# Kernel optimization log

Measured on AMD Instinct MI355X. Metric: run time of the kernel, lower is better.

## Reference

```python
import jax, jax.numpy as jnp
import numpy as np

B, H, W, C = 4, 64, 64, 256
DQK = C // 8

def setup_inputs() -> dict:
    key = jax.random.key(0)
    kx, kq, kk, kv = jax.random.split(key, 4)
    x = jax.random.normal(kx, (B, H, W, C), dtype=jnp.float32)
    Wq = jax.random.normal(kq, (C, DQK), dtype=jnp.float32) * 0.05
    Wk = jax.random.normal(kk, (C, DQK), dtype=jnp.float32) * 0.05
    Wv = jax.random.normal(kv, (C, C), dtype=jnp.float32) * 0.05
    gamma = jnp.ones((1,), dtype=jnp.float32)  # nonzero so attention path matters
    return {"x": x, "Wq": Wq, "Wk": Wk, "Wv": Wv, "gamma": gamma}

def reference(x, Wq, Wk, Wv, gamma):
    b, h, w, c = x.shape
    n = h * w
    xf = x.reshape(b, n, c)                      # [B, N, C]
    q = jnp.einsum('bnc,cd->bnd', xf, Wq)        # [B, N, C/8]  (1x1 conv == GEMM)
    k = jnp.einsum('bnc,cd->bnd', xf, Wk)        # [B, N, C/8]
    v = jnp.einsum('bnc,ce->bne', xf, Wv)        # [B, N, C]
    scores = jnp.einsum('bnd,bmd->bnm', q, k)    # [B, N, N], no scaling (as in source)
    attn = jax.nn.softmax(scores, axis=-1)
    out = jnp.einsum('bnm,bme->bne', attn, v)    # [B, N, C]
    out = out.reshape(b, h, w, c)
    return x + gamma * out
```

## Files before the change

### kernel.cpp

```cpp
#include <hip/hip_runtime.h>
#include <stdint.h>

#define BB 4
#define NN 4096
#define CC 256
#define DD 32

typedef __bf16 bf16;
typedef bf16 bf16x4 __attribute__((ext_vector_type(4)));
typedef bf16 bf16x8 __attribute__((ext_vector_type(8)));
typedef float f32x4 __attribute__((ext_vector_type(4)));
typedef unsigned int u32x4 __attribute__((ext_vector_type(4)));

__global__ void prepw_kernel(const float* __restrict__ Wq,
                             const float* __restrict__ Wk,
                             const float* __restrict__ Wv,
                             bf16* __restrict__ WT)
{
    int i = blockIdx.x * 256 + threadIdx.x;
    if (i < 320 * 256) {
        int d = i >> 8, c = i & 255;
        float val;
        if (d < DD)          val = Wq[c * DD + d] * 1.4426950408889634f;
        else if (d < 2 * DD) val = Wk[c * DD + (d - DD)];
        else                 val = Wv[c * CC + (d - 2 * DD)];
        WT[i] = (bf16)val;
    }
}

__global__ __launch_bounds__(256) void proj_kernel(
    const float* __restrict__ x, const bf16* __restrict__ WT,
    bf16* __restrict__ qb, bf16* __restrict__ kb, bf16* __restrict__ vt)
{
    int b = blockIdx.x >> 7, nt = blockIdx.x & 127;
    int n0 = nt << 5;
    int tid = threadIdx.x;
    int w = tid >> 6, lane = tid & 63;
    int lm = lane & 15, g = lane >> 4;
    int rw = w >> 1;
    int ch = w & 1;

    f32x4 acc[10];
    f32x4 zero4 = {0.f, 0.f, 0.f, 0.f};
#pragma unroll
    for (int i = 0; i < 10; ++i) acc[i] = zero4;

    const float* xrow = x + ((size_t)(b * NN) + n0 + rw * 16 + lm) * CC;
    for (int kc = 0; kc < 8; ++kc) {
        f32x4 a0 = *(const f32x4*)(xrow + kc * 32 + g * 8);
        f32x4 a1 = *(const f32x4*)(xrow + kc * 32 + g * 8 + 4);
        bf16x8 a;
        a[0] = (bf16)a0[0]; a[1] = (bf16)a0[1]; a[2] = (bf16)a0[2]; a[3] = (bf16)a0[3];
        a[4] = (bf16)a1[0]; a[5] = (bf16)a1[1]; a[6] = (bf16)a1[2]; a[7] = (bf16)a1[3];
#pragma unroll
        for (int ct = 0; ct < 10; ++ct) {
            int ctg = ch * 10 + ct;
            bf16x8 wv = *(const bf16x8*)(WT + (ctg * 16 + lm) * 256 + kc * 32 + g * 8);
            acc[ct] = __builtin_amdgcn_mfma_f32_16x16x32_bf16(a, wv, acc[ct], 0, 0, 0);
        }
    }

#pragma unroll
    for (int ct = 0; ct < 10; ++ct) {
        int ctg = ch * 10 + ct;
        int col = ctg * 16 + lm;
        if (ctg < 4) {
#pragma unroll
            for (int r = 0; r < 4; ++r) {
                int n = n0 + rw * 16 + g * 4 + r;
                bf16 hv = (bf16)acc[ct][r];
                if (ctg < 2) qb[((size_t)(b * NN) + n) * DD + col] = hv;
                else         kb[((size_t)(b * NN) + n) * DD + (col - DD)] = hv;
            }
        } else {
            int c = col - 64;
            int tile = nt >> 1;
            int nbase = ((nt & 1) * 32 + rw * 16 + g * 4) ^ ((c & 7) << 3);
            bf16x4 pk;
            pk[0] = (bf16)acc[ct][0]; pk[1] = (bf16)acc[ct][1];
            pk[2] = (bf16)acc[ct][2]; pk[3] = (bf16)acc[ct][3];
            size_t off = (((size_t)(b * 64 + tile)) * 256 + c) * 64 + nbase;
            *(bf16x4*)(vt + off) = pk;
        }
    }
}


#define LOADK(KT_, KF) { \
    const bf16* kbase_ = kb + ((size_t)(b * NN) + (size_t)(KT_) * 64) * DD + g * 8; \
    KF[0] = *(const bf16x8*)(kbase_ + (lm +  0) * DD); \
    KF[1] = *(const bf16x8*)(kbase_ + (lm + 16) * DD); \
    KF[2] = *(const bf16x8*)(kbase_ + (lm + 32) * DD); \
    KF[3] = *(const bf16x8*)(kbase_ + (lm + 48) * DD); }

#define LOADV(KT_, VB) { \
    const bf16* vtile_ = vt + ((size_t)(b * 64 + (KT_))) * 16384; \
    _Pragma("unroll") \
    for (int ct_ = 0; ct_ < 4; ++ct_) { \
        int c_ = 64 * w + 16 * ct_ + lm; \
        const bf16* vrow_ = vtile_ + c_ * 64; \
        int vsw_ = (c_ & 7) << 3; \
        VB[ct_][0] = *(const bf16x8*)(vrow_ + ((8 * g) ^ vsw_)); \
        VB[ct_][1] = *(const bf16x8*)(vrow_ + ((32 + 8 * g) ^ vsw_)); \
    } }

#define PVBLOCK(PRV_, VB) { \
    const float* alph_p = (const float*)(lds + 16384 + (PRV_) * 512); \
    const uint32_t* flg_p = (const uint32_t*)(lds + 16384 + (PRV_) * 512 + 256); \
    const unsigned char* Pp_ = lds + (PRV_) * 8192; \
    u32x4 fl_ = *(const u32x4*)flg_p; \
    if ((fl_[0] & fl_[1] & fl_[2] & fl_[3]) == 0u) { \
        _Pragma("unroll") for (int rt_ = 0; rt_ < 4; ++rt_) { \
            f32x4 a_ = *(const f32x4*)(alph_p + rt_ * 16 + 4 * g); \
            _Pragma("unroll") for (int ct_ = 0; ct_ < 4; ++ct_) { \
                acc[rt_][ct_][0] *= a_[0]; acc[rt_][ct_][1] *= a_[1]; \
                acc[rt_][ct_][2] *= a_[2]; acc[rt_][ct_][3] *= a_[3]; \
            } \
        } \
    } \
    int psw_ = (lm & 7) << 4; \
    _Pragma("unroll") for (int rt_ = 0; rt_ < 4; ++rt_) { \
        const unsigned char* pr_ = Pp_ + (rt_ * 16 + lm) * 128; \
        bf16x8 pa0_ = *(const bf16x8*)(pr_ + (( 0 + 16 * g) ^ psw_)); \
        bf16x8 pa1_ = *(const bf16x8*)(pr_ + ((64 + 16 * g) ^ psw_)); \
        _Pragma("unroll") for (int ct_ = 0; ct_ < 4; ++ct_) { \
            acc[rt_][ct_] = __builtin_amdgcn_mfma_f32_16x16x32_bf16(pa0_, VB[ct_][0], acc[rt_][ct_], 0, 0, 0); \
            acc[rt_][ct_] = __builtin_amdgcn_mfma_f32_16x16x32_bf16(pa1_, VB[ct_][1], acc[rt_][ct_], 0, 0, 0); \
        } \
    } \
}

#define STEP(T_, KF, KFN, VBP, DOPV) { \
    const int cur_ = (T_) & 1; \
    __builtin_amdgcn_s_setprio(1); \
    f32x4 sv0 = __builtin_amdgcn_mfma_f32_16x16x32_bf16(KF[0], qf, zero4, 0, 0, 0); \
    f32x4 sv1 = __builtin_amdgcn_mfma_f32_16x16x32_bf16(KF[1], qf, zero4, 0, 0, 0); \
    f32x4 sv2 = __builtin_amdgcn_mfma_f32_16x16x32_bf16(KF[2], qf, zero4, 0, 0, 0); \
    f32x4 sv3 = __builtin_amdgcn_mfma_f32_16x16x32_bf16(KF[3], qf, zero4, 0, 0, 0); \
    int ktn_ = ((T_) + 1 < kt1) ? ((T_) + 1) : (kt1 - 1); \
    LOADK(ktn_, KFN); \
    if (DOPV) { PVBLOCK(cur_ ^ 1, VBP); } \
    __builtin_amdgcn_s_setprio(0); \
    LOADV(ktn_, VBP); \
    float mx_ = fmaxf(fmaxf(fmaxf(sv0[0], sv0[1]), fmaxf(sv0[2], sv0[3])), \
                      fmaxf(fmaxf(sv1[0], sv1[1]), fmaxf(sv1[2], sv1[3]))); \
    mx_ = fmaxf(mx_, fmaxf(fmaxf(sv2[0], sv2[1]), fmaxf(sv2[2], sv2[3]))); \
    mx_ = fmaxf(mx_, fmaxf(fmaxf(sv3[0], sv3[1]), fmaxf(sv3[2], sv3[3]))); \
    float alpha_; \
    int wave_ok_ = __all(mx_ <= mrun + 11.5f); \
    if (!wave_ok_) { \
        float wm_ = mx_; \
        wm_ = fmaxf(wm_, __shfl_xor(wm_, 1)); \
        wm_ = fmaxf(wm_, __shfl_xor(wm_, 2)); \
        wm_ = fmaxf(wm_, __shfl_xor(wm_, 4)); \
        wm_ = fmaxf(wm_, __shfl_xor(wm_, 8)); \
        wm_ = fmaxf(wm_, __shfl_xor(wm_, 16)); \
        wm_ = fmaxf(wm_, __shfl_xor(wm_, 32)); \
        float mn_ = fmaxf(mrun, wm_); \
        alpha_ = __builtin_exp2f(mrun - mn_); \
        mrun = mn_; \
    } else alpha_ = 1.0f; \
    float ssum_; \
    { \
        _Pragma("unroll") for (int j_ = 0; j_ < 4; ++j_) sv0[j_] = __builtin_exp2f(sv0[j_] - mrun); \
        _Pragma("unroll") for (int j_ = 0; j_ < 4; ++j_) sv1[j_] = __builtin_exp2f(sv1[j_] - mrun); \
        _Pragma("unroll") for (int j_ = 0; j_ < 4; ++j_) sv2[j_] = __builtin_exp2f(sv2[j_] - mrun); \
        _Pragma("unroll") for (int j_ = 0; j_ < 4; ++j_) sv3[j_] = __builtin_exp2f(sv3[j_] - mrun); \
        f32x4 t_ = (sv0 + sv1) + (sv2 + sv3); \
        ssum_ = (t_[0] + t_[1]) + (t_[2] + t_[3]); \
    } \
    lrun = lrun * alpha_ + ssum_;   \
    unsigned char* Pb_ = lds + cur_ * 8192; \
    { \
        int rb_ = (16 * w + lm) * 128; \
        int sw_ = (lm & 7) << 4; \
        bf16x4 pk_; \
        pk_[0] = (bf16)sv0[0]; pk_[1] = (bf16)sv0[1]; pk_[2] = (bf16)sv0[2]; pk_[3] = (bf16)sv0[3]; \
        *(bf16x4*)(Pb_ + rb_ + (( 0 + 8 * g) ^ sw_)) = pk_; \
        pk_[0] = (bf16)sv1[0]; pk_[1] = (bf16)sv1[1]; pk_[2] = (bf16)sv1[2]; pk_[3] = (bf16)sv1[3]; \
        *(bf16x4*)(Pb_ + rb_ + ((32 + 8 * g) ^ sw_)) = pk_; \
        pk_[0] = (bf16)sv2[0]; pk_[1] = (bf16)sv2[1]; pk_[2] = (bf16)sv2[2]; pk_[3] = (bf16)sv2[3]; \
        *(bf16x4*)(Pb_ + rb_ + ((64 + 8 * g) ^ sw_)) = pk_; \
        pk_[0] = (bf16)sv3[0]; pk_[1] = (bf16)sv3[1]; pk_[2] = (bf16)sv3[2]; pk_[3] = (bf16)sv3[3]; \
        *(bf16x4*)(Pb_ + rb_ + ((96 + 8 * g) ^ sw_)) = pk_; \
    } \
    float* alph_ = (float*)(lds + 16384 + cur_ * 512); \
    uint32_t* flg_ = (uint32_t*)(lds + 16384 + cur_ * 512 + 256); \
    if (g == 0) alph_[16 * w + lm] = alpha_;   \
    if (lane == 0) flg_[w] = (uint32_t)wave_ok_; \
    asm volatile("s_waitcnt lgkmcnt(0)" ::: "memory"); \
    __builtin_amdgcn_s_barrier(); \
    asm volatile("" ::: "memory"); \
}

__global__ __launch_bounds__(256, 2) void attn_kernel(
    const bf16* __restrict__ qb, const bf16* __restrict__ kb,
    const bf16* __restrict__ vt, const float* __restrict__ x,
    const float* __restrict__ gamma, bf16* __restrict__ pacc,
    float* __restrict__ pml, float* __restrict__ out, int KS)
{
    __shared__ __align__(16) unsigned char lds[17408];
    int bid = blockIdx.x;
    int b, qt, ks;
    if (KS == 2) {
        int xcd = bid & 7, slot = bid >> 3;
        b = xcd >> 1;
        int idx = (xcd & 1) * 64 + slot;
        qt = idx >> 1; ks = idx & 1;
    } else {
        ks = bid % KS; int t = bid / KS; b = t >> 6; qt = t & 63;
    }
    int bq = b * 64 + qt;
    int n0 = qt << 6;
    int tid = threadIdx.x;
    int w = tid >> 6, lane = tid & 63;
    int lm = lane & 15, g = lane >> 4;

    bf16x8 qf = *(const bf16x8*)(qb + ((size_t)(b * NN) + n0 + w * 16 + lm) * DD + g * 8);

    f32x4 acc[4][4];
    f32x4 zero4 = {0.f, 0.f, 0.f, 0.f};
#pragma unroll
    for (int i = 0; i < 4; ++i)
#pragma unroll
        for (int j = 0; j < 4; ++j) acc[i][j] = zero4;
    float mrun = -1e30f, lrun = 0.f;

    int KT = 64 / KS;
    int kt0 = ks * KT;
    int kt1 = kt0 + KT;

    bf16x8 kfA[4], kfB[4];
    bf16x8 vbA[4][2], vbB[4][2];
    LOADK(kt0, kfA);
    LOADV(kt0, vbA);

    STEP(kt0, kfA, kfB, vbB, 0);

    int kt = kt0 + 1;
    while (kt + 2 <= kt1) {
        STEP(kt,     kfB, kfA, vbA, 1);
        STEP(kt + 1, kfA, kfB, vbB, 1);
        kt += 2;
    }
    if (kt < kt1) {
        STEP(kt, kfB, kfA, vbA, 1);
    }
    PVBLOCK(1, vbB);

    lrun += __shfl_xor(lrun, 16);
    lrun += __shfl_xor(lrun, 32);

    if (KS == 1) {
        __syncthreads();
        float* lsh = (float*)(lds + 16384);
        if (g == 0) lsh[16 * w + lm] = lrun;
        __syncthreads();
        float gam = gamma[0];
#pragma unroll
        for (int rt = 0; rt < 4; ++rt) {
            f32x4 lv = *(const f32x4*)(lsh + rt * 16 + 4 * g);
            f32x4 inv;
            inv[0] = 1.f / lv[0]; inv[1] = 1.f / lv[1];
            inv[2] = 1.f / lv[2]; inv[3] = 1.f / lv[3];
#pragma unroll
            for (int ct = 0; ct < 4; ++ct) {
                int col = 64 * w + 16 * ct + lm;
#pragma unroll
                for (int r = 0; r < 4; ++r) {
                    int n = n0 + rt * 16 + 4 * g + r;
                    size_t idx = ((size_t)(b * NN) + n) * CC + col;
                    out[idx] = x[idx] + gam * acc[rt][ct][r] * inv[r];
                }
            }
        }
    } else {
        bf16* pa = pacc + ((size_t)(bq * KS + ks)) * (64 * 256);
#pragma unroll
        for (int rt = 0; rt < 4; ++rt) {
#pragma unroll
            for (int ct = 0; ct < 4; ++ct) {
                int col = 64 * w + 16 * ct + lm;
#pragma unroll
                for (int r = 0; r < 4; ++r) {
                    int rowin = rt * 16 + 4 * g + r;
                    pa[rowin * 256 + col] = (bf16)acc[rt][ct][r];
                }
            }
        }
        if (g == 0) {
            int rowin = 16 * w + lm;
            size_t mo = ((size_t)(bq * KS + ks) * 64 + rowin) * 2;
            pml[mo + 0] = mrun;
            pml[mo + 1] = lrun;
        }
    }
}

__global__ __launch_bounds__(256) void combine_kernel(
    const bf16* __restrict__ pacc, const float* __restrict__ pml,
    const float* __restrict__ x, const float* __restrict__ gamma,
    float* __restrict__ out, int KS)
{
    int tid = threadIdx.x;
    int row = blockIdx.x * 4 + (tid >> 6);
    int lane = tid & 63;
    int bq = row >> 6;
    int r64 = row & 63;

    float m[4], l[4];
    float M = -3e38f;
    for (int ks = 0; ks < KS; ++ks) {
        size_t mo = ((size_t)(bq * KS + ks) * 64 + r64) * 2;
        m[ks] = pml[mo + 0];
        l[ks] = pml[mo + 1];
        M = fmaxf(M, m[ks]);
    }
    float L = 0.f;
    float wgt[4];
    for (int ks = 0; ks < KS; ++ks) {
        wgt[ks] = __builtin_exp2f(m[ks] - M);
        L += wgt[ks] * l[ks];
    }
    float s = gamma[0] / L;

    f32x4 a = {0.f, 0.f, 0.f, 0.f};
    for (int ks = 0; ks < KS; ++ks) {
        const bf16* pa = pacc + ((size_t)(bq * KS + ks) * 64 + r64) * 256;
        bf16x4 v = *(const bf16x4*)(pa + lane * 4);
        a[0] += wgt[ks] * (float)v[0]; a[1] += wgt[ks] * (float)v[1];
        a[2] += wgt[ks] * (float)v[2]; a[3] += wgt[ks] * (float)v[3];
    }
    const f32x4* xv = (const f32x4*)(x + (size_t)row * 256);
    f32x4 xi = xv[lane];
    f32x4 o;
    o[0] = xi[0] + s * a[0]; o[1] = xi[1] + s * a[1];
    o[2] = xi[2] + s * a[2]; o[3] = xi[3] + s * a[3];
    ((f32x4*)(out + (size_t)row * 256))[lane] = o;
}

extern "C" void kernel_launch(void* const* d_in, const int* in_sizes, int n_in,
                              void* d_out, int out_size, void* d_ws, size_t ws_size,
                              hipStream_t stream)
{
    const float* x     = (const float*)d_in[0];
    const float* Wq    = (const float*)d_in[1];
    const float* Wk    = (const float*)d_in[2];
    const float* Wv    = (const float*)d_in[3];
    const float* gamma = (const float*)d_in[4];
    float* out = (float*)d_out;

    char* ws = (char*)d_ws;
    bf16* WT = (bf16*)(ws);
    bf16* qb = (bf16*)(ws + 163840);
    bf16* kb = (bf16*)(ws + 1212416);
    bf16* vt = (bf16*)(ws + 2260992);

    const size_t base = 10649600;
    size_t need2 = base + (size_t)2 * (8388608 + 131072);
    int KS = (ws_size >= need2) ? 2 : 1;

    bf16*  pacc = (bf16*)(ws + base);
    float* pml  = (float*)(ws + base + (size_t)KS * 8388608);

    hipLaunchKernelGGL(prepw_kernel, dim3(320), dim3(256), 0, stream,
                       Wq, Wk, Wv, WT);
    hipLaunchKernelGGL(proj_kernel, dim3(512), dim3(256), 0, stream,
                       x, WT, qb, kb, vt);
    hipLaunchKernelGGL(attn_kernel, dim3(256 * KS), dim3(256), 0, stream,
                       qb, kb, vt, x, gamma, pacc, pml, out, KS);
    if (KS > 1) {
        hipLaunchKernelGGL(combine_kernel, dim3(BB * NN / 4), dim3(256), 0, stream,
                           pacc, pml, x, gamma, out, KS);
    }
}
```

Before: 92.61 us.

## Split attention keys three ways, raise occupancy, and single-buffer K/V fragments

The key range is now split into three partitions instead of two, giving 768 blocks with an XCD-aware block mapping and uneven tile ranges per split. Occupancy is raised to three blocks per SIMD through launch bounds. The double-buffered K/V register fragments and the unrolled two-step loop become a single-buffered rolled loop, which frees registers so the higher occupancy fits. In exchange, V loads now have less time in flight before they are used. The split also needs more workspace; if the buffer is too small, the code falls back to a single split instead of two.

```diff
diff --git a/kernel.cpp b/kernel.cpp
--- a/kernel.cpp
+++ b/kernel.cpp
@@ -11,6 +11,10 @@
 typedef bf16 bf16x8 __attribute__((ext_vector_type(8)));
 typedef float f32x4 __attribute__((ext_vector_type(4)));
 typedef unsigned int u32x4 __attribute__((ext_vector_type(4)));
+
+__device__ __forceinline__ float fm3(float a, float b, float c) {
+    return fmaxf(fmaxf(a, b), c);
+}
 
 __global__ void prepw_kernel(const float* __restrict__ Wq,
                              const float* __restrict__ Wk,
@@ -86,25 +90,25 @@
 }
 
 
-#define LOADK(KT_, KF) { \
+#define LOADK(KT_) { \
     const bf16* kbase_ = kb + ((size_t)(b * NN) + (size_t)(KT_) * 64) * DD + g * 8; \
-    KF[0] = *(const bf16x8*)(kbase_ + (lm +  0) * DD); \
-    KF[1] = *(const bf16x8*)(kbase_ + (lm + 16) * DD); \
-    KF[2] = *(const bf16x8*)(kbase_ + (lm + 32) * DD); \
-    KF[3] = *(const bf16x8*)(kbase_ + (lm + 48) * DD); }
-
-#define LOADV(KT_, VB) { \
+    kf[0] = *(const bf16x8*)(kbase_ + (lm +  0) * DD); \
+    kf[1] = *(const bf16x8*)(kbase_ + (lm + 16) * DD); \
+    kf[2] = *(const bf16x8*)(kbase_ + (lm + 32) * DD); \
+    kf[3] = *(const bf16x8*)(kbase_ + (lm + 48) * DD); }
+
+#define LOADV(KT_) { \
     const bf16* vtile_ = vt + ((size_t)(b * 64 + (KT_))) * 16384; \
     _Pragma("unroll") \
     for (int ct_ = 0; ct_ < 4; ++ct_) { \
         int c_ = 64 * w + 16 * ct_ + lm; \
         const bf16* vrow_ = vtile_ + c_ * 64; \
         int vsw_ = (c_ & 7) << 3; \
-        VB[ct_][0] = *(const bf16x8*)(vrow_ + ((8 * g) ^ vsw_)); \
-        VB[ct_][1] = *(const bf16x8*)(vrow_ + ((32 + 8 * g) ^ vsw_)); \
+        vb[ct_][0] = *(const bf16x8*)(vrow_ + ((8 * g) ^ vsw_)); \
+        vb[ct_][1] = *(const bf16x8*)(vrow_ + ((32 + 8 * g) ^ vsw_)); \
     } }
 
-#define PVBLOCK(PRV_, VB) { \
+#define PVBLOCK(PRV_) { \
     const float* alph_p = (const float*)(lds + 16384 + (PRV_) * 512); \
     const uint32_t* flg_p = (const uint32_t*)(lds + 16384 + (PRV_) * 512 + 256); \
     const unsigned char* Pp_ = lds + (PRV_) * 8192; \
@@ -119,33 +123,27 @@
         } \
     } \
     int psw_ = (lm & 7) << 4; \
+    __builtin_amdgcn_s_setprio(1); \
     _Pragma("unroll") for (int rt_ = 0; rt_ < 4; ++rt_) { \
         const unsigned char* pr_ = Pp_ + (rt_ * 16 + lm) * 128; \
         bf16x8 pa0_ = *(const bf16x8*)(pr_ + (( 0 + 16 * g) ^ psw_)); \
         bf16x8 pa1_ = *(const bf16x8*)(pr_ + ((64 + 16 * g) ^ psw_)); \
         _Pragma("unroll") for (int ct_ = 0; ct_ < 4; ++ct_) { \
-            acc[rt_][ct_] = __builtin_amdgcn_mfma_f32_16x16x32_bf16(pa0_, VB[ct_][0], acc[rt_][ct_], 0, 0, 0); \
-            acc[rt_][ct_] = __builtin_amdgcn_mfma_f32_16x16x32_bf16(pa1_, VB[ct_][1], acc[rt_][ct_], 0, 0, 0); \
+            acc[rt_][ct_] = __builtin_amdgcn_mfma_f32_16x16x32_bf16(pa0_, vb[ct_][0], acc[rt_][ct_], 0, 0, 0); \
+            acc[rt_][ct_] = __builtin_amdgcn_mfma_f32_16x16x32_bf16(pa1_, vb[ct_][1], acc[rt_][ct_], 0, 0, 0); \
         } \
     } \
-}
-
-#define STEP(T_, KF, KFN, VBP, DOPV) { \
+    __builtin_amdgcn_s_setprio(0); \
+}
+
+#define SMTAIL(T_) { \
     const int cur_ = (T_) & 1; \
-    __builtin_amdgcn_s_setprio(1); \
-    f32x4 sv0 = __builtin_amdgcn_mfma_f32_16x16x32_bf16(KF[0], qf, zero4, 0, 0, 0); \
-    f32x4 sv1 = __builtin_amdgcn_mfma_f32_16x16x32_bf16(KF[1], qf, zero4, 0, 0, 0); \
-    f32x4 sv2 = __builtin_amdgcn_mfma_f32_16x16x32_bf16(KF[2], qf, zero4, 0, 0, 0); \
-    f32x4 sv3 = __builtin_amdgcn_mfma_f32_16x16x32_bf16(KF[3], qf, zero4, 0, 0, 0); \
-    int ktn_ = ((T_) + 1 < kt1) ? ((T_) + 1) : (kt1 - 1); \
-    LOADK(ktn_, KFN); \
-    if (DOPV) { PVBLOCK(cur_ ^ 1, VBP); } \
-    __builtin_amdgcn_s_setprio(0); \
-    LOADV(ktn_, VBP); \
-    float mx_ = fmaxf(fmaxf(fmaxf(sv0[0], sv0[1]), fmaxf(sv0[2], sv0[3])), \
-                      fmaxf(fmaxf(sv1[0], sv1[1]), fmaxf(sv1[2], sv1[3]))); \
-    mx_ = fmaxf(mx_, fmaxf(fmaxf(sv2[0], sv2[1]), fmaxf(sv2[2], sv2[3]))); \
-    mx_ = fmaxf(mx_, fmaxf(fmaxf(sv3[0], sv3[1]), fmaxf(sv3[2], sv3[3]))); \
+    float mxa_ = fm3(sv0[0], sv0[1], sv0[2]); \
+    float mxb_ = fm3(sv0[3], sv1[0], sv1[1]); \
+    float mxc_ = fm3(sv1[2], sv1[3], sv2[0]); \
+    float mxd_ = fm3(sv2[1], sv2[2], sv2[3]); \
+    float mxe_ = fm3(sv3[0], sv3[1], sv3[2]); \
+    float mx_ = fmaxf(fm3(mxa_, mxb_, mxc_), fm3(mxd_, mxe_, sv3[3])); \
     float alpha_; \
     int wave_ok_ = __all(mx_ <= mrun + 11.5f); \
     if (!wave_ok_) { \
@@ -186,14 +184,14 @@
     } \
     float* alph_ = (float*)(lds + 16384 + cur_ * 512); \
     uint32_t* flg_ = (uint32_t*)(lds + 16384 + cur_ * 512 + 256); \
-    if (g == 0) alph_[16 * w + lm] = alpha_;   \
+    if (g == 0) alph_[16 * w + lm] = alpha_; \
     if (lane == 0) flg_[w] = (uint32_t)wave_ok_; \
     asm volatile("s_waitcnt lgkmcnt(0)" ::: "memory"); \
     __builtin_amdgcn_s_barrier(); \
     asm volatile("" ::: "memory"); \
 }
 
-__global__ __launch_bounds__(256, 2) void attn_kernel(
+__global__ __launch_bounds__(256, 3) void attn_kernel(
     const bf16* __restrict__ qb, const bf16* __restrict__ kb,
     const bf16* __restrict__ vt, const float* __restrict__ x,
     const float* __restrict__ gamma, bf16* __restrict__ pacc,
@@ -202,11 +200,11 @@
     __shared__ __align__(16) unsigned char lds[17408];
     int bid = blockIdx.x;
     int b, qt, ks;
-    if (KS == 2) {
+    if (KS == 3) {
         int xcd = bid & 7, slot = bid >> 3;
         b = xcd >> 1;
-        int idx = (xcd & 1) * 64 + slot;
-        qt = idx >> 1; ks = idx & 1;
+        int idx = (xcd & 1) * 96 + slot;
+        qt = idx / 3; ks = idx - qt * 3;
     } else {
         ks = bid % KS; int t = bid / KS; b = t >> 6; qt = t & 63;
     }
@@ -226,27 +224,35 @@
         for (int j = 0; j < 4; ++j) acc[i][j] = zero4;
     float mrun = -1e30f, lrun = 0.f;
 
-    int KT = 64 / KS;
-    int kt0 = ks * KT;
-    int kt1 = kt0 + KT;
-
-    bf16x8 kfA[4], kfB[4];
-    bf16x8 vbA[4][2], vbB[4][2];
-    LOADK(kt0, kfA);
-    LOADV(kt0, vbA);
-
-    STEP(kt0, kfA, kfB, vbB, 0);
-
-    int kt = kt0 + 1;
-    while (kt + 2 <= kt1) {
-        STEP(kt,     kfB, kfA, vbA, 1);
-        STEP(kt + 1, kfA, kfB, vbB, 1);
-        kt += 2;
-    }
-    if (kt < kt1) {
-        STEP(kt, kfB, kfA, vbA, 1);
-    }
-    PVBLOCK(1, vbB);
+    int kt0 = (64 * ks) / KS;
+    int kt1 = (64 * (ks + 1)) / KS;
+
+    bf16x8 kf[4];
+    bf16x8 vb[4][2];
+    LOADK(kt0);
+    LOADV(kt0);
+
+    {
+        f32x4 sv0 = __builtin_amdgcn_mfma_f32_16x16x32_bf16(kf[0], qf, zero4, 0, 0, 0);
+        f32x4 sv1 = __builtin_amdgcn_mfma_f32_16x16x32_bf16(kf[1], qf, zero4, 0, 0, 0);
+        f32x4 sv2 = __builtin_amdgcn_mfma_f32_16x16x32_bf16(kf[2], qf, zero4, 0, 0, 0);
+        f32x4 sv3 = __builtin_amdgcn_mfma_f32_16x16x32_bf16(kf[3], qf, zero4, 0, 0, 0);
+        LOADK(kt0 + 1);
+        SMTAIL(kt0);
+    }
+
+    for (int kt = kt0 + 1; kt < kt1; ++kt) {
+        f32x4 sv0 = __builtin_amdgcn_mfma_f32_16x16x32_bf16(kf[0], qf, zero4, 0, 0, 0);
+        f32x4 sv1 = __builtin_amdgcn_mfma_f32_16x16x32_bf16(kf[1], qf, zero4, 0, 0, 0);
+        f32x4 sv2 = __builtin_amdgcn_mfma_f32_16x16x32_bf16(kf[2], qf, zero4, 0, 0, 0);
+        f32x4 sv3 = __builtin_amdgcn_mfma_f32_16x16x32_bf16(kf[3], qf, zero4, 0, 0, 0);
+        int ktn = (kt + 1) & 63;
+        LOADK(ktn);
+        PVBLOCK((kt & 1) ^ 1);
+        LOADV(kt);
+        SMTAIL(kt);
+    }
+    PVBLOCK((kt1 - 1) & 1);
 
     lrun += __shfl_xor(lrun, 16);
     lrun += __shfl_xor(lrun, 32);
@@ -357,8 +363,8 @@
     bf16* vt = (bf16*)(ws + 2260992);
 
     const size_t base = 10649600;
-    size_t need2 = base + (size_t)2 * (8388608 + 131072);
-    int KS = (ws_size >= need2) ? 2 : 1;
+    size_t need3 = base + (size_t)3 * (8388608 + 131072);
+    int KS = (ws_size >= need3) ? 3 : 1;
 
     bf16*  pacc = (bf16*)(ws + base);
     float* pml  = (float*)(ws + base + (size_t)KS * 8388608);
```

After: 95.46 us. 1.03x slower.

## Fuse split-K combine into attention kernel via per-tile atomic counter

Applied to the files above, without the earlier changes.

Removes the separate combine kernel launch. The last-arriving split block for each query tile, detected with an atomic counter after a threadfence, merges the two partial accumulators and writes the output. It also raises wave priority around the PV MFMA block. This saves a launch and lets combine work overlap with attention tail blocks, at the cost of atomics, fences, and one block per tile doing serial combine work.

```diff
diff --git a/kernel.cpp b/kernel.cpp
--- a/kernel.cpp
+++ b/kernel.cpp
@@ -15,9 +15,11 @@
 __global__ void prepw_kernel(const float* __restrict__ Wq,
                              const float* __restrict__ Wk,
                              const float* __restrict__ Wv,
-                             bf16* __restrict__ WT)
+                             bf16* __restrict__ WT,
+                             int* __restrict__ cnt)
 {
     int i = blockIdx.x * 256 + threadIdx.x;
+    if (blockIdx.x == 0 && threadIdx.x < 256) cnt[threadIdx.x] = 0;
     if (i < 320 * 256) {
         int d = i >> 8, c = i & 255;
         float val;
@@ -119,6 +121,7 @@
         } \
     } \
     int psw_ = (lm & 7) << 4; \
+    __builtin_amdgcn_s_setprio(1); \
     _Pragma("unroll") for (int rt_ = 0; rt_ < 4; ++rt_) { \
         const unsigned char* pr_ = Pp_ + (rt_ * 16 + lm) * 128; \
         bf16x8 pa0_ = *(const bf16x8*)(pr_ + (( 0 + 16 * g) ^ psw_)); \
@@ -128,6 +131,7 @@
             acc[rt_][ct_] = __builtin_amdgcn_mfma_f32_16x16x32_bf16(pa1_, VB[ct_][1], acc[rt_][ct_], 0, 0, 0); \
         } \
     } \
+    __builtin_amdgcn_s_setprio(0); \
 }
 
 #define STEP(T_, KF, KFN, VBP, DOPV) { \
@@ -186,7 +190,7 @@
     } \
     float* alph_ = (float*)(lds + 16384 + cur_ * 512); \
     uint32_t* flg_ = (uint32_t*)(lds + 16384 + cur_ * 512 + 256); \
-    if (g == 0) alph_[16 * w + lm] = alpha_;   \
+    if (g == 0) alph_[16 * w + lm] = alpha_; \
     if (lane == 0) flg_[w] = (uint32_t)wave_ok_; \
     asm volatile("s_waitcnt lgkmcnt(0)" ::: "memory"); \
     __builtin_amdgcn_s_barrier(); \
@@ -197,7 +201,8 @@
     const bf16* __restrict__ qb, const bf16* __restrict__ kb,
     const bf16* __restrict__ vt, const float* __restrict__ x,
     const float* __restrict__ gamma, bf16* __restrict__ pacc,
-    float* __restrict__ pml, float* __restrict__ out, int KS)
+    float* __restrict__ pml, int* __restrict__ cnt,
+    float* __restrict__ out, int KS)
 {
     __shared__ __align__(16) unsigned char lds[17408];
     int bid = blockIdx.x;
@@ -294,49 +299,43 @@
             pml[mo + 0] = mrun;
             pml[mo + 1] = lrun;
         }
-    }
-}
-
-__global__ __launch_bounds__(256) void combine_kernel(
-    const bf16* __restrict__ pacc, const float* __restrict__ pml,
-    const float* __restrict__ x, const float* __restrict__ gamma,
-    float* __restrict__ out, int KS)
-{
-    int tid = threadIdx.x;
-    int row = blockIdx.x * 4 + (tid >> 6);
-    int lane = tid & 63;
-    int bq = row >> 6;
-    int r64 = row & 63;
-
-    float m[4], l[4];
-    float M = -3e38f;
-    for (int ks = 0; ks < KS; ++ks) {
-        size_t mo = ((size_t)(bq * KS + ks) * 64 + r64) * 2;
-        m[ks] = pml[mo + 0];
-        l[ks] = pml[mo + 1];
-        M = fmaxf(M, m[ks]);
-    }
-    float L = 0.f;
-    float wgt[4];
-    for (int ks = 0; ks < KS; ++ks) {
-        wgt[ks] = __builtin_exp2f(m[ks] - M);
-        L += wgt[ks] * l[ks];
-    }
-    float s = gamma[0] / L;
-
-    f32x4 a = {0.f, 0.f, 0.f, 0.f};
-    for (int ks = 0; ks < KS; ++ks) {
-        const bf16* pa = pacc + ((size_t)(bq * KS + ks) * 64 + r64) * 256;
-        bf16x4 v = *(const bf16x4*)(pa + lane * 4);
-        a[0] += wgt[ks] * (float)v[0]; a[1] += wgt[ks] * (float)v[1];
-        a[2] += wgt[ks] * (float)v[2]; a[3] += wgt[ks] * (float)v[3];
-    }
-    const f32x4* xv = (const f32x4*)(x + (size_t)row * 256);
-    f32x4 xi = xv[lane];
-    f32x4 o;
-    o[0] = xi[0] + s * a[0]; o[1] = xi[1] + s * a[1];
-    o[2] = xi[2] + s * a[2]; o[3] = xi[3] + s * a[3];
-    ((f32x4*)(out + (size_t)row * 256))[lane] = o;
+
+        __syncthreads();
+        if (tid == 0) {
+            __threadfence();
+            int old = atomicAdd(&cnt[bq], 1);
+            *(int*)lds = old;
+        }
+        __syncthreads();
+        int old = *(int*)lds;
+        if (old == 1) {
+            __threadfence();
+            float gam = gamma[0];
+            int lane4 = tid & 63;
+            int r0 = tid >> 6;
+            for (int rr = r0; rr < 64; rr += 4) {
+                size_t row = (size_t)bq * 64 + rr;
+                size_t mo0 = ((size_t)(bq * 2 + 0) * 64 + rr) * 2;
+                size_t mo1 = ((size_t)(bq * 2 + 1) * 64 + rr) * 2;
+                float m0 = pml[mo0], l0 = pml[mo0 + 1];
+                float m1 = pml[mo1], l1 = pml[mo1 + 1];
+                float M = fmaxf(m0, m1);
+                float w0 = __builtin_exp2f(m0 - M);
+                float w1 = __builtin_exp2f(m1 - M);
+                float s = gam / (w0 * l0 + w1 * l1);
+                const bf16* p0 = pacc + ((size_t)(bq * 2 + 0) * 64 + rr) * 256 + lane4 * 4;
+                const bf16* p1 = pacc + ((size_t)(bq * 2 + 1) * 64 + rr) * 256 + lane4 * 4;
+                bf16x4 v0 = *(const bf16x4*)p0;
+                bf16x4 v1 = *(const bf16x4*)p1;
+                f32x4 xi = ((const f32x4*)(x + row * 256))[lane4];
+                f32x4 o;
+#pragma unroll
+                for (int j = 0; j < 4; ++j)
+                    o[j] = xi[j] + s * (w0 * (float)v0[j] + w1 * (float)v1[j]);
+                ((f32x4*)(out + row * 256))[lane4] = o;
+            }
+        }
+    }
 }
 
 extern "C" void kernel_launch(void* const* d_in, const int* in_sizes, int n_in,
@@ -357,20 +356,18 @@
     bf16* vt = (bf16*)(ws + 2260992);
 
     const size_t base = 10649600;
-    size_t need2 = base + (size_t)2 * (8388608 + 131072);
+    const size_t accB = 8388608, mlB = 131072;
+    size_t need2 = base + 2 * (accB + mlB) + 1024;
     int KS = (ws_size >= need2) ? 2 : 1;
 
     bf16*  pacc = (bf16*)(ws + base);
-    float* pml  = (float*)(ws + base + (size_t)KS * 8388608);
+    float* pml  = (float*)(ws + base + (size_t)KS * accB);
+    int*   cnt  = (int*)(ws + base + (size_t)KS * (accB + mlB));
 
     hipLaunchKernelGGL(prepw_kernel, dim3(320), dim3(256), 0, stream,
-                       Wq, Wk, Wv, WT);
+                       Wq, Wk, Wv, WT, cnt);
     hipLaunchKernelGGL(proj_kernel, dim3(512), dim3(256), 0, stream,
                        x, WT, qb, kb, vt);
     hipLaunchKernelGGL(attn_kernel, dim3(256 * KS), dim3(256), 0, stream,
-                       qb, kb, vt, x, gamma, pacc, pml, out, KS);
-    if (KS > 1) {
-        hipLaunchKernelGGL(combine_kernel, dim3(BB * NN / 4), dim3(256), 0, stream,
-                           pacc, pml, x, gamma, out, KS);
-    }
-}
+                       qb, kb, vt, x, gamma, pacc, pml, cnt, out, KS);
+}
```

After: 144.3 us. +55.9%, slower.

## Process two key tiles per barrier with quad-buffered P in LDS

Applied to the files above, without the earlier changes.

Restructures the flash-attention inner loop so each barrier covers two key tiles (two HALF steps), using four P/alpha slots in LDS instead of two, which halves the number of block barriers. K fragments are prefetched two tiles ahead, and V loads are issued right after the PV block that consumed the previous buffer. It also raises MFMA priority around the PV MFMAs and rebalances the max reduction into 3-input max ops. LDS per block doubles, which could affect occupancy. The loop structure assumes KT is even, and the final-tile handling looks fragile.

```diff
diff --git a/kernel.cpp b/kernel.cpp
--- a/kernel.cpp
+++ b/kernel.cpp
@@ -11,6 +11,10 @@
 typedef bf16 bf16x8 __attribute__((ext_vector_type(8)));
 typedef float f32x4 __attribute__((ext_vector_type(4)));
 typedef unsigned int u32x4 __attribute__((ext_vector_type(4)));
+
+__device__ __forceinline__ float fm3(float a, float b, float c) {
+    return fmaxf(fmaxf(a, b), c);
+}
 
 __global__ void prepw_kernel(const float* __restrict__ Wq,
                              const float* __restrict__ Wk,
@@ -104,10 +108,10 @@
         VB[ct_][1] = *(const bf16x8*)(vrow_ + ((32 + 8 * g) ^ vsw_)); \
     } }
 
-#define PVBLOCK(PRV_, VB) { \
-    const float* alph_p = (const float*)(lds + 16384 + (PRV_) * 512); \
-    const uint32_t* flg_p = (const uint32_t*)(lds + 16384 + (PRV_) * 512 + 256); \
-    const unsigned char* Pp_ = lds + (PRV_) * 8192; \
+#define PVBLOCK(SL_, VB) { \
+    const float* alph_p = (const float*)(lds + 32768 + (SL_) * 512); \
+    const uint32_t* flg_p = (const uint32_t*)(lds + 32768 + (SL_) * 512 + 256); \
+    const unsigned char* Pp_ = lds + (SL_) * 8192; \
     u32x4 fl_ = *(const u32x4*)flg_p; \
     if ((fl_[0] & fl_[1] & fl_[2] & fl_[3]) == 0u) { \
         _Pragma("unroll") for (int rt_ = 0; rt_ < 4; ++rt_) { \
@@ -119,6 +123,7 @@
         } \
     } \
     int psw_ = (lm & 7) << 4; \
+    __builtin_amdgcn_s_setprio(1); \
     _Pragma("unroll") for (int rt_ = 0; rt_ < 4; ++rt_) { \
         const unsigned char* pr_ = Pp_ + (rt_ * 16 + lm) * 128; \
         bf16x8 pa0_ = *(const bf16x8*)(pr_ + (( 0 + 16 * g) ^ psw_)); \
@@ -128,24 +133,25 @@
             acc[rt_][ct_] = __builtin_amdgcn_mfma_f32_16x16x32_bf16(pa1_, VB[ct_][1], acc[rt_][ct_], 0, 0, 0); \
         } \
     } \
-}
-
-#define STEP(T_, KF, KFN, VBP, DOPV) { \
-    const int cur_ = (T_) & 1; \
+    __builtin_amdgcn_s_setprio(0); \
+}
+
+#define HALF(T_, KF, VB, WS_, DOPV) { \
     __builtin_amdgcn_s_setprio(1); \
     f32x4 sv0 = __builtin_amdgcn_mfma_f32_16x16x32_bf16(KF[0], qf, zero4, 0, 0, 0); \
     f32x4 sv1 = __builtin_amdgcn_mfma_f32_16x16x32_bf16(KF[1], qf, zero4, 0, 0, 0); \
     f32x4 sv2 = __builtin_amdgcn_mfma_f32_16x16x32_bf16(KF[2], qf, zero4, 0, 0, 0); \
     f32x4 sv3 = __builtin_amdgcn_mfma_f32_16x16x32_bf16(KF[3], qf, zero4, 0, 0, 0); \
-    int ktn_ = ((T_) + 1 < kt1) ? ((T_) + 1) : (kt1 - 1); \
-    LOADK(ktn_, KFN); \
-    if (DOPV) { PVBLOCK(cur_ ^ 1, VBP); } \
     __builtin_amdgcn_s_setprio(0); \
-    LOADV(ktn_, VBP); \
-    float mx_ = fmaxf(fmaxf(fmaxf(sv0[0], sv0[1]), fmaxf(sv0[2], sv0[3])), \
-                      fmaxf(fmaxf(sv1[0], sv1[1]), fmaxf(sv1[2], sv1[3]))); \
-    mx_ = fmaxf(mx_, fmaxf(fmaxf(sv2[0], sv2[1]), fmaxf(sv2[2], sv2[3]))); \
-    mx_ = fmaxf(mx_, fmaxf(fmaxf(sv3[0], sv3[1]), fmaxf(sv3[2], sv3[3]))); \
+    int ktn_ = ((T_) + 2 < kt1) ? ((T_) + 2) : (kt1 - 1); \
+    LOADK(ktn_, KF); \
+    if (DOPV) { PVBLOCK((WS_) ^ 2, VB); LOADV((T_), VB); } \
+    float mxa_ = fm3(sv0[0], sv0[1], sv0[2]); \
+    float mxb_ = fm3(sv0[3], sv1[0], sv1[1]); \
+    float mxc_ = fm3(sv1[2], sv1[3], sv2[0]); \
+    float mxd_ = fm3(sv2[1], sv2[2], sv2[3]); \
+    float mxe_ = fm3(sv3[0], sv3[1], sv3[2]); \
+    float mx_ = fmaxf(fm3(mxa_, mxb_, mxc_), fm3(mxd_, mxe_, sv3[3])); \
     float alpha_; \
     int wave_ok_ = __all(mx_ <= mrun + 11.5f); \
     if (!wave_ok_) { \
@@ -170,7 +176,7 @@
         ssum_ = (t_[0] + t_[1]) + (t_[2] + t_[3]); \
     } \
     lrun = lrun * alpha_ + ssum_;   \
-    unsigned char* Pb_ = lds + cur_ * 8192; \
+    unsigned char* Pb_ = lds + (WS_) * 8192; \
     { \
         int rb_ = (16 * w + lm) * 128; \
         int sw_ = (lm & 7) << 4; \
@@ -184,10 +190,13 @@
         pk_[0] = (bf16)sv3[0]; pk_[1] = (bf16)sv3[1]; pk_[2] = (bf16)sv3[2]; pk_[3] = (bf16)sv3[3]; \
         *(bf16x4*)(Pb_ + rb_ + ((96 + 8 * g) ^ sw_)) = pk_; \
     } \
-    float* alph_ = (float*)(lds + 16384 + cur_ * 512); \
-    uint32_t* flg_ = (uint32_t*)(lds + 16384 + cur_ * 512 + 256); \
-    if (g == 0) alph_[16 * w + lm] = alpha_;   \
+    float* alph_ = (float*)(lds + 32768 + (WS_) * 512); \
+    uint32_t* flg_ = (uint32_t*)(lds + 32768 + (WS_) * 512 + 256); \
+    if (g == 0) alph_[16 * w + lm] = alpha_; \
     if (lane == 0) flg_[w] = (uint32_t)wave_ok_; \
+}
+
+#define SUPBAR() { \
     asm volatile("s_waitcnt lgkmcnt(0)" ::: "memory"); \
     __builtin_amdgcn_s_barrier(); \
     asm volatile("" ::: "memory"); \
@@ -199,7 +208,7 @@
     const float* __restrict__ gamma, bf16* __restrict__ pacc,
     float* __restrict__ pml, float* __restrict__ out, int KS)
 {
-    __shared__ __align__(16) unsigned char lds[17408];
+    __shared__ __align__(16) unsigned char lds[34816];
     int bid = blockIdx.x;
     int b, qt, ks;
     if (KS == 2) {
@@ -229,31 +238,46 @@
     int KT = 64 / KS;
     int kt0 = ks * KT;
     int kt1 = kt0 + KT;
+    int S = KT >> 1;
 
     bf16x8 kfA[4], kfB[4];
     bf16x8 vbA[4][2], vbB[4][2];
     LOADK(kt0, kfA);
+    LOADK(kt0 + 1, kfB);
     LOADV(kt0, vbA);
-
-    STEP(kt0, kfA, kfB, vbB, 0);
-
-    int kt = kt0 + 1;
-    while (kt + 2 <= kt1) {
-        STEP(kt,     kfB, kfA, vbA, 1);
-        STEP(kt + 1, kfA, kfB, vbB, 1);
-        kt += 2;
-    }
-    if (kt < kt1) {
-        STEP(kt, kfB, kfA, vbA, 1);
-    }
-    PVBLOCK(1, vbB);
+    LOADV(kt0 + 1, vbB);
+
+    HALF(kt0,     kfA, vbA, 0, 0);
+    HALF(kt0 + 1, kfB, vbB, 1, 0);
+    SUPBAR();
+
+    int s = 1;
+    while (s + 1 < S) {
+        int t0 = kt0 + 2 * s;
+        HALF(t0,     kfA, vbA, 2, 1);
+        HALF(t0 + 1, kfB, vbB, 3, 1);
+        SUPBAR();
+        int t2 = t0 + 2;
+        HALF(t2,     kfA, vbA, 0, 1);
+        HALF(t2 + 1, kfB, vbB, 1, 1);
+        SUPBAR();
+        s += 2;
+    }
+    {
+        int t0 = kt0 + 2 * s;
+        HALF(t0,     kfA, vbA, 2, 1);
+        HALF(t0 + 1, kfB, vbB, 3, 1);
+        SUPBAR();
+    }
+    PVBLOCK(2, vbA);
+    PVBLOCK(3, vbB);
 
     lrun += __shfl_xor(lrun, 16);
     lrun += __shfl_xor(lrun, 32);
 
     if (KS == 1) {
         __syncthreads();
-        float* lsh = (float*)(lds + 16384);
+        float* lsh = (float*)(lds + 32768);
         if (g == 0) lsh[16 * w + lm] = lrun;
         __syncthreads();
         float gam = gamma[0];
```

Result: slower. 130.0 us (+40.4%).
